# Kernel optimization log

Hardware: AMD Instinct MI355X
Metric: run time of the kernel (lower is better)

Reference implementation:

```python
import jax, jax.numpy as jnp
import numpy as np


def _gcn_conv(x, src, dst, W, b, n_nodes):
    """PyG GCNConv: out = D^-1/2 (A+I) D^-1/2 (x @ W) + b, sym norm with self-loops."""
    loop = jnp.arange(n_nodes, dtype=src.dtype)
    s = jnp.concatenate([src, loop])  # sources incl self-loops
    d = jnp.concatenate([dst, loop])  # destinations incl self-loops
    ones = jnp.ones(d.shape[0], dtype=x.dtype)
    deg = jax.ops.segment_sum(ones, d, num_segments=n_nodes)
    dinv = jnp.where(deg > 0, jax.lax.rsqrt(deg), 0.0)
    norm = dinv[s] * dinv[d]  # [E+N]
    h = x @ W  # dense transform first (in>=out channels), [N, H]
    msg = h[s] * norm[:, None]  # gather + scale, [E+N, H]
    out = jax.ops.segment_sum(msg, d, num_segments=n_nodes)  # scatter-add
    return out + b


def setup_inputs() -> dict:
    N, E, C_IN, C_H = 50000, 640000, 128, 128
    key = jax.random.key(0)
    k_x, k_e, k_w1, k_w2 = jax.random.split(key, 4)
    x = jax.random.normal(k_x, (N, C_IN), dtype=jnp.float32)
    edge_index = jax.random.randint(k_e, (2, E), 0, N, dtype=jnp.int64)
    # Glorot-style init for GCN weights, zero bias (PyG defaults)
    W1 = jax.random.normal(k_w1, (C_IN, C_H), dtype=jnp.float32) * (1.0 / np.sqrt(C_IN))
    b1 = jnp.zeros((C_H,), dtype=jnp.float32)
    W2 = jax.random.normal(k_w2, (C_H, C_H), dtype=jnp.float32) * (1.0 / np.sqrt(C_H))
    b2 = jnp.zeros((C_H,), dtype=jnp.float32)
    return {"x": x, "edge_index": edge_index, "W1": W1, "b1": b1, "W2": W2, "b2": b2}


def reference(x, edge_index, W1, b1, W2, b2):
    n_nodes = x.shape[0]
    src, dst = edge_index[0], edge_index[1]
    h = jax.nn.relu(_gcn_conv(x, src, dst, W1, b1, n_nodes))
    # dropout p=0.5 is identity in eval mode (training=False)
    h = jax.nn.relu(_gcn_conv(h, src, dst, W2, b2, n_nodes))
    return h
```

## Files before the change

### kernel.cpp

```cpp
#include <hip/hip_runtime.h>
#include <hip/hip_bf16.h>
#include <cstdint>

#define CH 128
#define NB 512
#define SCHUNK 4096

typedef __attribute__((ext_vector_type(8))) short short8;
typedef __attribute__((ext_vector_type(4))) float f32x4;

union FragU {
  uint4 u;
  short8 s;
  ushort h[8];
};

__device__ __forceinline__ float bf_lo(uint32_t u) { return __uint_as_float(u << 16); }
__device__ __forceinline__ float bf_hi(uint32_t u) { return __uint_as_float(u & 0xffff0000u); }
__device__ __forceinline__ uint32_t f2bf(float f) {
  uint32_t u = __float_as_uint(f);
  u += 0x7fff + ((u >> 16) & 1);
  return u >> 16;
}

__global__ __launch_bounds__(256) void k_hist2(const int* __restrict__ dst, int* __restrict__ counts,
                                               int E, int nblk) {
  __shared__ int sh[NB];
  int t = threadIdx.x, blk = blockIdx.x;
  for (int i = t; i < NB; i += 256) sh[i] = 0;
  __syncthreads();
  int base = blk * SCHUNK, lim = min(base + SCHUNK, E);
  for (int i = base + t; i < lim; i += 256) atomicAdd(&sh[dst[i] >> 7], 1);
  __syncthreads();
  for (int i = t; i < NB; i += 256) counts[i * nblk + blk] = sh[i];
}

__global__ __launch_bounds__(1024) void k_scan1(const int* __restrict__ in, int* __restrict__ excl,
                                                int* __restrict__ blocksum, int n) {
  __shared__ int sd[1024];
  int tid = threadIdx.x;
  int i = blockIdx.x * 1024 + tid;
  int v = (i < n) ? in[i] : 0;
  int x = v;
  sd[tid] = x;
  __syncthreads();
  for (int off = 1; off < 1024; off <<= 1) {
    int t = (tid >= off) ? sd[tid - off] : 0;
    __syncthreads();
    x += t;
    sd[tid] = x;
    __syncthreads();
  }
  if (i < n) excl[i] = x - v;
  if (tid == 1023) blocksum[blockIdx.x] = x;
}

__global__ void k_scan2b(int* __restrict__ bs, int nb) {
  __shared__ int sh[128];
  int t = threadIdx.x;
  int v = (t < nb) ? bs[t] : 0;
  sh[t] = v;
  __syncthreads();
  for (int off = 1; off < 128; off <<= 1) {
    int add = (t >= off) ? sh[t - off] : 0;
    __syncthreads();
    sh[t] += add;
    __syncthreads();
  }
  if (t < nb) bs[t] = sh[t] - v;
}

__global__ __launch_bounds__(256) void k_scan3b(int* __restrict__ excl, const int* __restrict__ boff,
                                                int* __restrict__ bbase, int total, int nblk, int E) {
  int i = blockIdx.x * 256 + threadIdx.x;
  if (i < total) {
    int val = excl[i] + boff[i >> 10];
    excl[i] = val;
    if (i % nblk == 0) bbase[i / nblk] = val;
  }
  if (i == 0) bbase[NB] = E;
}

__global__ __launch_bounds__(256) void k_scatter3(const int* __restrict__ src, const int* __restrict__ dst,
                                                  const int* __restrict__ excl, uint32_t* __restrict__ packed,
                                                  int E, int nblk) {
  __shared__ int lcur[NB];
  int t = threadIdx.x, blk = blockIdx.x;
  for (int i = t; i < NB; i += 256) lcur[i] = excl[i * nblk + blk];
  __syncthreads();
  int base = blk * SCHUNK, lim = min(base + SCHUNK, E);
  for (int i = base + t; i < lim; i += 256) {
    int d = dst[i], s = src[i];
    int slot = atomicAdd(&lcur[d >> 7], 1);
    packed[slot] = (uint32_t)s | ((uint32_t)(d & 127) << 16);
  }
}

__global__ __launch_bounds__(256) void k_bucket(const uint32_t* __restrict__ packed, const int* __restrict__ bbase,
                                                int* __restrict__ csr_src, int* __restrict__ row_ptr,
                                                float* __restrict__ dinv, int N, int E, int nb) {
  __shared__ int hist[128];
  __shared__ int scan[128];
  __shared__ int cur[128];
  int b = blockIdx.x;
  int t = threadIdx.x;
  int base = bbase[b], end = bbase[b + 1];
  if (t < 128) hist[t] = 0;
  __syncthreads();
  for (int i = base + t; i < end; i += 256)
    atomicAdd(&hist[packed[i] >> 16], 1);
  __syncthreads();
  int v = (t < 128) ? hist[t] : 0;
  if (t < 128) scan[t] = v;
  __syncthreads();
  for (int off = 1; off < 128; off <<= 1) {
    int add = (t < 128 && t >= off) ? scan[t - off] : 0;
    __syncthreads();
    if (t < 128) scan[t] += add;
    __syncthreads();
  }
  if (t < 128) {
    int excl = scan[t] - v;
    cur[t] = excl;
    int node = b * 128 + t;
    if (node < N) {
      row_ptr[node] = base + excl;
      dinv[node] = rsqrtf((float)(v + 1));
    }
    if (b == nb - 1 && t == 0) row_ptr[N] = E;
  }
  __syncthreads();
  for (int i = base + t; i < end; i += 256) {
    uint32_t p = packed[i];
    int slot = atomicAdd(&cur[p >> 16], 1);
    csr_src[base + slot] = (int)(p & 0xffffu);
  }
}

__global__ __launch_bounds__(256) void k_wpack(const float* __restrict__ W1, const float* __restrict__ W2,
                                               ushort* __restrict__ buf) {
  int which = blockIdx.x >> 6;
  int idx = (blockIdx.x & 63) * 256 + threadIdx.x;
  const float* W = which ? W2 : W1;
  ushort* hi = buf + which * 32768;
  ushort* lo = hi + 16384;
  int k = idx >> 7, n = idx & 127;
  float w = W[idx];
  uint32_t hb = f2bf(w);
  uint32_t lb = f2bf(w - bf_lo(hb));
  int j = n >> 4, t = k >> 5, ln = (n & 15) | (((k >> 3) & 3) << 4), i = k & 7;
  int p = (j * 4 + t) * 512 + ln * 8 + i;
  hi[p] = (ushort)hb;
  lo[p] = (ushort)lb;
}

template <typename TA, bool OUT_BF16>
__global__ __launch_bounds__(256) void k_gemm_mfma(const TA* __restrict__ A,
                                                   const ushort* __restrict__ wpack,
                                                   void* __restrict__ Cp, int n) {
  const int lane = threadIdx.x & 63;
  const int gwave = (blockIdx.x * 256 + threadIdx.x) >> 6;
  const int rb = gwave * 32;
  if (rb >= n) return;
  const int lrow = lane & 15, lgrp = lane >> 4;
  const uint4* whi4 = (const uint4*)wpack;
  const uint4* wlo4 = (const uint4*)(wpack + 16384);

  const int r0 = rb + lrow, r1 = rb + 16 + lrow;
  const bool v0 = r0 < n, v1 = r1 < n;
  const int rc0 = v0 ? r0 : 0, rc1 = v1 ? r1 : 0;

  f32x4 acc0[8] = {};
  f32x4 acc1[8] = {};
  const uint4 zz = make_uint4(0, 0, 0, 0);

#pragma unroll
  for (int t = 0; t < 4; ++t) {
    FragU a0h, a0l, a1h, a1l;
    if constexpr (sizeof(TA) == 4) {
      const float* ap0 = (const float*)A + (size_t)rc0 * CH + t * 32 + lgrp * 8;
      const float* ap1 = (const float*)A + (size_t)rc1 * CH + t * 32 + lgrp * 8;
      float4 xa = *(const float4*)ap0, xb = *(const float4*)(ap0 + 4);
      float4 ya = *(const float4*)ap1, yb = *(const float4*)(ap1 + 4);
      float xv[8] = {xa.x, xa.y, xa.z, xa.w, xb.x, xb.y, xb.z, xb.w};
      float yv[8] = {ya.x, ya.y, ya.z, ya.w, yb.x, yb.y, yb.z, yb.w};
#pragma unroll
      for (int i = 0; i < 8; ++i) {
        uint32_t h0 = f2bf(xv[i]);
        a0h.h[i] = (ushort)h0;
        a0l.h[i] = (ushort)f2bf(xv[i] - bf_lo(h0));
        uint32_t h1 = f2bf(yv[i]);
        a1h.h[i] = (ushort)h1;
        a1l.h[i] = (ushort)f2bf(yv[i] - bf_lo(h1));
      }
      if (!v0) { a0h.u = zz; a0l.u = zz; }
      if (!v1) { a1h.u = zz; a1l.u = zz; }
    } else {
      a0h.u = v0 ? *(const uint4*)((const ushort*)A + (size_t)rc0 * CH + t * 32 + lgrp * 8) : zz;
      a1h.u = v1 ? *(const uint4*)((const ushort*)A + (size_t)rc1 * CH + t * 32 + lgrp * 8) : zz;
    }
#pragma unroll
    for (int j = 0; j < 8; ++j) {
      FragU wh, wl;
      wh.u = whi4[(j * 4 + t) * 64 + lane];
      wl.u = wlo4[(j * 4 + t) * 64 + lane];
      acc0[j] = __builtin_amdgcn_mfma_f32_16x16x32_bf16(wh.s, a0h.s, acc0[j], 0, 0, 0);
      acc0[j] = __builtin_amdgcn_mfma_f32_16x16x32_bf16(wl.s, a0h.s, acc0[j], 0, 0, 0);
      acc1[j] = __builtin_amdgcn_mfma_f32_16x16x32_bf16(wh.s, a1h.s, acc1[j], 0, 0, 0);
      acc1[j] = __builtin_amdgcn_mfma_f32_16x16x32_bf16(wl.s, a1h.s, acc1[j], 0, 0, 0);
      if constexpr (sizeof(TA) == 4) {
        acc0[j] = __builtin_amdgcn_mfma_f32_16x16x32_bf16(wh.s, a0l.s, acc0[j], 0, 0, 0);
        acc1[j] = __builtin_amdgcn_mfma_f32_16x16x32_bf16(wh.s, a1l.s, acc1[j], 0, 0, 0);
      }
    }
  }

  if (v0) {
#pragma unroll
    for (int j = 0; j < 8; ++j) {
      if constexpr (OUT_BF16) {
        uint2 o;
        o.x = f2bf(acc0[j][0]) | (f2bf(acc0[j][1]) << 16);
        o.y = f2bf(acc0[j][2]) | (f2bf(acc0[j][3]) << 16);
        *(uint2*)&((ushort*)Cp)[(size_t)r0 * CH + j * 16 + lgrp * 4] = o;
      } else {
        float4 o = make_float4(acc0[j][0], acc0[j][1], acc0[j][2], acc0[j][3]);
        *(float4*)&((float*)Cp)[(size_t)r0 * CH + j * 16 + lgrp * 4] = o;
      }
    }
  }
  if (v1) {
#pragma unroll
    for (int j = 0; j < 8; ++j) {
      if constexpr (OUT_BF16) {
        uint2 o;
        o.x = f2bf(acc1[j][0]) | (f2bf(acc1[j][1]) << 16);
        o.y = f2bf(acc1[j][2]) | (f2bf(acc1[j][3]) << 16);
        *(uint2*)&((ushort*)Cp)[(size_t)r1 * CH + j * 16 + lgrp * 4] = o;
      } else {
        float4 o = make_float4(acc1[j][0], acc1[j][1], acc1[j][2], acc1[j][3]);
        *(float4*)&((float*)Cp)[(size_t)r1 * CH + j * 16 + lgrp * 4] = o;
      }
    }
  }
}

template <bool OUT_BF16>
__global__ __launch_bounds__(256) void k_agg(const ushort* __restrict__ h, const int* __restrict__ row_ptr,
                                             const int* __restrict__ csr_src, const float* __restrict__ dinv,
                                             const float* __restrict__ b, void* __restrict__ outp, int n) {
  int v = (blockIdx.x * 256 + threadIdx.x) >> 6;
  int lane = threadIdx.x & 63;
  if (v >= n) return;
  v = __builtin_amdgcn_readfirstlane(v);
  float dv = dinv[v];
  uint32_t us = *(const uint32_t*)&h[(size_t)v * CH + 2 * lane];
  float self = dv * dv;
  float acc0 = bf_lo(us) * self;
  float acc1 = bf_hi(us) * self;
  int j = row_ptr[v], end = row_ptr[v + 1];
  for (; j + 3 < end; j += 4) {
    int s0 = csr_src[j], s1 = csr_src[j + 1], s2 = csr_src[j + 2], s3 = csr_src[j + 3];
    float w0 = dinv[s0] * dv, w1 = dinv[s1] * dv, w2 = dinv[s2] * dv, w3 = dinv[s3] * dv;
    uint32_t u0 = *(const uint32_t*)&h[(size_t)s0 * CH + 2 * lane];
    uint32_t u1 = *(const uint32_t*)&h[(size_t)s1 * CH + 2 * lane];
    uint32_t u2 = *(const uint32_t*)&h[(size_t)s2 * CH + 2 * lane];
    uint32_t u3 = *(const uint32_t*)&h[(size_t)s3 * CH + 2 * lane];
    acc0 += bf_lo(u0) * w0; acc1 += bf_hi(u0) * w0;
    acc0 += bf_lo(u1) * w1; acc1 += bf_hi(u1) * w1;
    acc0 += bf_lo(u2) * w2; acc1 += bf_hi(u2) * w2;
    acc0 += bf_lo(u3) * w3; acc1 += bf_hi(u3) * w3;
  }
  for (; j < end; ++j) {
    int s0 = csr_src[j];
    float w0 = dinv[s0] * dv;
    uint32_t u0 = *(const uint32_t*)&h[(size_t)s0 * CH + 2 * lane];
    acc0 += bf_lo(u0) * w0; acc1 += bf_hi(u0) * w0;
  }
  float2 bb = *(const float2*)&b[2 * lane];
  acc0 = fmaxf(acc0 + bb.x, 0.f);
  acc1 = fmaxf(acc1 + bb.y, 0.f);
  if constexpr (OUT_BF16) {
    ((uint32_t*)outp)[(size_t)v * 64 + lane] = f2bf(acc0) | (f2bf(acc1) << 16);
  } else {
    ((float2*)outp)[(size_t)v * 64 + lane] = make_float2(acc0, acc1);
  }
}


extern "C" void kernel_launch(void* const* d_in, const int* in_sizes, int n_in,
                              void* d_out, int out_size, void* d_ws, size_t ws_size,
                              hipStream_t stream) {
  const float* x  = (const float*)d_in[0];
  const int*   ei = (const int*)d_in[1];
  const float* W1 = (const float*)d_in[2];
  const float* b1 = (const float*)d_in[3];
  const float* W2 = (const float*)d_in[4];
  const float* b2 = (const float*)d_in[5];
  float* out = (float*)d_out;

  const int N = in_sizes[0] / CH;
  const int E = in_sizes[1] / 2;
  const int* src = ei;
  const int* dst = ei + E;
  const int nb = (N + 127) / 128;
  const int nblk = (E + SCHUNK - 1) / SCHUNK;
  const int total = NB * nblk;
  const int nsb = (total + 1023) / 1024;

  char* ws = (char*)d_ws;
  size_t off = 0;
  auto alloc = [&](size_t bytes) -> void* {
    void* p = ws + off;
    off += (bytes + 255) & ~(size_t)255;
    return p;
  };
  int*      counts  = (int*)alloc((size_t)total * 4);
  int*      blocksum= (int*)alloc(128 * 4);
  int*      bbase   = (int*)alloc((NB + 1) * 4);
  uint32_t* packed  = (uint32_t*)alloc((size_t)E * 4);
  int*      row_ptr = (int*)alloc((size_t)(N + 1) * 4);
  int*      csr_src = (int*)alloc((size_t)E * 4);
  float*    dinv    = (float*)alloc((size_t)N * 4);
  ushort*   wpack   = (ushort*)alloc(4 * 16384 * 2);
  ushort*   h       = (ushort*)alloc((size_t)N * CH * 2);
  ushort*   y1      = (ushort*)alloc((size_t)N * CH * 2);
  (void)ws_size;

  k_hist2<<<nblk, 256, 0, stream>>>(dst, counts, E, nblk);
  k_scan1<<<nsb, 1024, 0, stream>>>(counts, counts, blocksum, total);
  k_scan2b<<<1, 128, 0, stream>>>(blocksum, nsb);
  k_scan3b<<<(total + 255) / 256, 256, 0, stream>>>(counts, blocksum, bbase, total, nblk, E);
  k_scatter3<<<nblk, 256, 0, stream>>>(src, dst, counts, packed, E, nblk);
  k_bucket<<<nb, 256, 0, stream>>>(packed, bbase, csr_src, row_ptr, dinv, N, E, nb);
  k_wpack<<<128, 256, 0, stream>>>(W1, W2, wpack);

  const int waves = (N + 31) / 32;
  const int gG = (waves + 3) / 4;
  const int gA = (N + 3) / 4;

  k_gemm_mfma<float, true><<<gG, 256, 0, stream>>>(x, wpack, h, N);
  k_agg<true><<<gA, 256, 0, stream>>>(h, row_ptr, csr_src, dinv, b1, y1, N);
  k_gemm_mfma<ushort, true><<<gG, 256, 0, stream>>>(y1, wpack + 32768, h, N);
  k_agg<false><<<gA, 256, 0, stream>>>(h, row_ptr, csr_src, dinv, b2, out, N);
}
```

Measured before the change: 131.8 us.

## Fuse layer-1 aggregation with layer-2 GEMM, prescale by dinv, merge prep kernels

Fuses the first aggregation with the second GEMM through shared memory, so the intermediate y1 never goes to global memory and one launch disappears. The GEMM epilogue now multiplies rows by dinv, which removes the per-edge dinv gather in aggregation; the aggregation loop is unrolled by 8 with wave-uniform bounds. The three scan kernels become a single-block scan, and weight packing is merged into the histogram launch. Risks: the fused kernel has only 32 nodes per block, so aggregation latency may be exposed, and the single-block scan is serial per thread.

```diff
diff --git a/kernel.cpp b/kernel.cpp
--- a/kernel.cpp
+++ b/kernel.cpp
@@ -23,10 +23,30 @@
   return u >> 16;
 }
 
-__global__ __launch_bounds__(256) void k_hist2(const int* __restrict__ dst, int* __restrict__ counts,
-                                               int E, int nblk) {
+__global__ __launch_bounds__(256) void k_histw(const int* __restrict__ dst, int* __restrict__ counts,
+                                               int E, int nblk,
+                                               const float* __restrict__ W1, const float* __restrict__ W2,
+                                               ushort* __restrict__ wbuf) {
+  int blk = blockIdx.x;
+  if (blk >= nblk) {
+    int bb = blk - nblk;
+    int which = bb >> 6;
+    int idx = (bb & 63) * 256 + threadIdx.x;
+    const float* W = which ? W2 : W1;
+    ushort* hi = wbuf + which * 32768;
+    ushort* lo = hi + 16384;
+    int k = idx >> 7, n = idx & 127;
+    float w = W[idx];
+    uint32_t hb = f2bf(w);
+    uint32_t lb = f2bf(w - bf_lo(hb));
+    int j = n >> 4, t = k >> 5, ln = (n & 15) | (((k >> 3) & 3) << 4), i = k & 7;
+    int p = (j * 4 + t) * 512 + ln * 8 + i;
+    hi[p] = (ushort)hb;
+    lo[p] = (ushort)lb;
+    return;
+  }
   __shared__ int sh[NB];
-  int t = threadIdx.x, blk = blockIdx.x;
+  int t = threadIdx.x;
   for (int i = t; i < NB; i += 256) sh[i] = 0;
   __syncthreads();
   int base = blk * SCHUNK, lim = min(base + SCHUNK, E);
@@ -35,50 +55,30 @@
   for (int i = t; i < NB; i += 256) counts[i * nblk + blk] = sh[i];
 }
 
-__global__ __launch_bounds__(1024) void k_scan1(const int* __restrict__ in, int* __restrict__ excl,
-                                                int* __restrict__ blocksum, int n) {
-  __shared__ int sd[1024];
-  int tid = threadIdx.x;
-  int i = blockIdx.x * 1024 + tid;
-  int v = (i < n) ? in[i] : 0;
-  int x = v;
-  sd[tid] = x;
+__global__ __launch_bounds__(1024) void k_scan_all(int* __restrict__ counts, int* __restrict__ bbase,
+                                                   int total, int nblk, int E) {
+  __shared__ int ssum[1024];
+  int t = threadIdx.x;
+  int chunk = (total + 1023) / 1024;
+  int lo = t * chunk, hi = min(lo + chunk, total);
+  int s = 0;
+  for (int i = lo; i < hi; ++i) s += counts[i];
+  ssum[t] = s;
   __syncthreads();
   for (int off = 1; off < 1024; off <<= 1) {
-    int t = (tid >= off) ? sd[tid - off] : 0;
+    int add = (t >= off) ? ssum[t - off] : 0;
     __syncthreads();
-    x += t;
-    sd[tid] = x;
+    ssum[t] += add;
     __syncthreads();
   }
-  if (i < n) excl[i] = x - v;
-  if (tid == 1023) blocksum[blockIdx.x] = x;
-}
-
-__global__ void k_scan2b(int* __restrict__ bs, int nb) {
-  __shared__ int sh[128];
-  int t = threadIdx.x;
-  int v = (t < nb) ? bs[t] : 0;
-  sh[t] = v;
-  __syncthreads();
-  for (int off = 1; off < 128; off <<= 1) {
-    int add = (t >= off) ? sh[t - off] : 0;
-    __syncthreads();
-    sh[t] += add;
-    __syncthreads();
-  }
-  if (t < nb) bs[t] = sh[t] - v;
-}
-
-__global__ __launch_bounds__(256) void k_scan3b(int* __restrict__ excl, const int* __restrict__ boff,
-                                                int* __restrict__ bbase, int total, int nblk, int E) {
-  int i = blockIdx.x * 256 + threadIdx.x;
-  if (i < total) {
-    int val = excl[i] + boff[i >> 10];
-    excl[i] = val;
-    if (i % nblk == 0) bbase[i / nblk] = val;
-  }
-  if (i == 0) bbase[NB] = E;
+  int run = ssum[t] - s;
+  for (int i = lo; i < hi; ++i) {
+    int v = counts[i];
+    counts[i] = run;
+    if (i % nblk == 0) bbase[i / nblk] = run;
+    run += v;
+  }
+  if (t == 0) bbase[NB] = E;
 }
 
 __global__ __launch_bounds__(256) void k_scatter3(const int* __restrict__ src, const int* __restrict__ dst,
@@ -137,27 +137,10 @@
   }
 }
 
-__global__ __launch_bounds__(256) void k_wpack(const float* __restrict__ W1, const float* __restrict__ W2,
-                                               ushort* __restrict__ buf) {
-  int which = blockIdx.x >> 6;
-  int idx = (blockIdx.x & 63) * 256 + threadIdx.x;
-  const float* W = which ? W2 : W1;
-  ushort* hi = buf + which * 32768;
-  ushort* lo = hi + 16384;
-  int k = idx >> 7, n = idx & 127;
-  float w = W[idx];
-  uint32_t hb = f2bf(w);
-  uint32_t lb = f2bf(w - bf_lo(hb));
-  int j = n >> 4, t = k >> 5, ln = (n & 15) | (((k >> 3) & 3) << 4), i = k & 7;
-  int p = (j * 4 + t) * 512 + ln * 8 + i;
-  hi[p] = (ushort)hb;
-  lo[p] = (ushort)lb;
-}
-
-template <typename TA, bool OUT_BF16>
-__global__ __launch_bounds__(256) void k_gemm_mfma(const TA* __restrict__ A,
+__global__ __launch_bounds__(256) void k_gemm_mfma(const float* __restrict__ A,
                                                    const ushort* __restrict__ wpack,
-                                                   void* __restrict__ Cp, int n) {
+                                                   const float* __restrict__ dinv,
+                                                   ushort* __restrict__ Cp, int n) {
   const int lane = threadIdx.x & 63;
   const int gwave = (blockIdx.x * 256 + threadIdx.x) >> 6;
   const int rb = gwave * 32;
@@ -177,28 +160,23 @@
 #pragma unroll
   for (int t = 0; t < 4; ++t) {
     FragU a0h, a0l, a1h, a1l;
-    if constexpr (sizeof(TA) == 4) {
-      const float* ap0 = (const float*)A + (size_t)rc0 * CH + t * 32 + lgrp * 8;
-      const float* ap1 = (const float*)A + (size_t)rc1 * CH + t * 32 + lgrp * 8;
-      float4 xa = *(const float4*)ap0, xb = *(const float4*)(ap0 + 4);
-      float4 ya = *(const float4*)ap1, yb = *(const float4*)(ap1 + 4);
-      float xv[8] = {xa.x, xa.y, xa.z, xa.w, xb.x, xb.y, xb.z, xb.w};
-      float yv[8] = {ya.x, ya.y, ya.z, ya.w, yb.x, yb.y, yb.z, yb.w};
-#pragma unroll
-      for (int i = 0; i < 8; ++i) {
-        uint32_t h0 = f2bf(xv[i]);
-        a0h.h[i] = (ushort)h0;
-        a0l.h[i] = (ushort)f2bf(xv[i] - bf_lo(h0));
-        uint32_t h1 = f2bf(yv[i]);
-        a1h.h[i] = (ushort)h1;
-        a1l.h[i] = (ushort)f2bf(yv[i] - bf_lo(h1));
-      }
-      if (!v0) { a0h.u = zz; a0l.u = zz; }
-      if (!v1) { a1h.u = zz; a1l.u = zz; }
-    } else {
-      a0h.u = v0 ? *(const uint4*)((const ushort*)A + (size_t)rc0 * CH + t * 32 + lgrp * 8) : zz;
-      a1h.u = v1 ? *(const uint4*)((const ushort*)A + (size_t)rc1 * CH + t * 32 + lgrp * 8) : zz;
-    }
+    const float* ap0 = A + (size_t)rc0 * CH + t * 32 + lgrp * 8;
+    const float* ap1 = A + (size_t)rc1 * CH + t * 32 + lgrp * 8;
+    float4 xa = *(const float4*)ap0, xb = *(const float4*)(ap0 + 4);
+    float4 ya = *(const float4*)ap1, yb = *(const float4*)(ap1 + 4);
+    float xv[8] = {xa.x, xa.y, xa.z, xa.w, xb.x, xb.y, xb.z, xb.w};
+    float yv[8] = {ya.x, ya.y, ya.z, ya.w, yb.x, yb.y, yb.z, yb.w};
+#pragma unroll
+    for (int i = 0; i < 8; ++i) {
+      uint32_t h0 = f2bf(xv[i]);
+      a0h.h[i] = (ushort)h0;
+      a0l.h[i] = (ushort)f2bf(xv[i] - bf_lo(h0));
+      uint32_t h1 = f2bf(yv[i]);
+      a1h.h[i] = (ushort)h1;
+      a1l.h[i] = (ushort)f2bf(yv[i] - bf_lo(h1));
+    }
+    if (!v0) { a0h.u = zz; a0l.u = zz; }
+    if (!v1) { a1h.u = zz; a1l.u = zz; }
 #pragma unroll
     for (int j = 0; j < 8; ++j) {
       FragU wh, wl;
@@ -206,85 +184,149 @@
       wl.u = wlo4[(j * 4 + t) * 64 + lane];
       acc0[j] = __builtin_amdgcn_mfma_f32_16x16x32_bf16(wh.s, a0h.s, acc0[j], 0, 0, 0);
       acc0[j] = __builtin_amdgcn_mfma_f32_16x16x32_bf16(wl.s, a0h.s, acc0[j], 0, 0, 0);
+      acc0[j] = __builtin_amdgcn_mfma_f32_16x16x32_bf16(wh.s, a0l.s, acc0[j], 0, 0, 0);
       acc1[j] = __builtin_amdgcn_mfma_f32_16x16x32_bf16(wh.s, a1h.s, acc1[j], 0, 0, 0);
       acc1[j] = __builtin_amdgcn_mfma_f32_16x16x32_bf16(wl.s, a1h.s, acc1[j], 0, 0, 0);
-      if constexpr (sizeof(TA) == 4) {
-        acc0[j] = __builtin_amdgcn_mfma_f32_16x16x32_bf16(wh.s, a0l.s, acc0[j], 0, 0, 0);
-        acc1[j] = __builtin_amdgcn_mfma_f32_16x16x32_bf16(wh.s, a1l.s, acc1[j], 0, 0, 0);
+      acc1[j] = __builtin_amdgcn_mfma_f32_16x16x32_bf16(wh.s, a1l.s, acc1[j], 0, 0, 0);
+    }
+  }
+
+  if (v0) {
+    float dv = dinv[r0];
+#pragma unroll
+    for (int j = 0; j < 8; ++j) {
+      uint2 o;
+      o.x = f2bf(acc0[j][0] * dv) | (f2bf(acc0[j][1] * dv) << 16);
+      o.y = f2bf(acc0[j][2] * dv) | (f2bf(acc0[j][3] * dv) << 16);
+      *(uint2*)&Cp[(size_t)r0 * CH + j * 16 + lgrp * 4] = o;
+    }
+  }
+  if (v1) {
+    float dv = dinv[r1];
+#pragma unroll
+    for (int j = 0; j < 8; ++j) {
+      uint2 o;
+      o.x = f2bf(acc1[j][0] * dv) | (f2bf(acc1[j][1] * dv) << 16);
+      o.y = f2bf(acc1[j][2] * dv) | (f2bf(acc1[j][3] * dv) << 16);
+      *(uint2*)&Cp[(size_t)r1 * CH + j * 16 + lgrp * 4] = o;
+    }
+  }
+}
+
+__device__ __forceinline__ void agg_node(const uint32_t* __restrict__ hp, const int* __restrict__ row_ptr,
+                                         const int* __restrict__ csr, int v, int lane,
+                                         float& a0, float& a1) {
+  uint32_t self = hp[(size_t)v * 64 + lane];
+  float acc0 = bf_lo(self), acc1 = bf_hi(self);
+  int j = __builtin_amdgcn_readfirstlane(row_ptr[v]);
+  int end = __builtin_amdgcn_readfirstlane(row_ptr[v + 1]);
+  for (; j + 7 < end; j += 8) {
+    int s[8];
+#pragma unroll
+    for (int k = 0; k < 8; ++k) s[k] = csr[j + k];
+    uint32_t u[8];
+#pragma unroll
+    for (int k = 0; k < 8; ++k) u[k] = hp[(size_t)s[k] * 64 + lane];
+#pragma unroll
+    for (int k = 0; k < 8; ++k) { acc0 += bf_lo(u[k]); acc1 += bf_hi(u[k]); }
+  }
+  for (; j < end; ++j) {
+    uint32_t u = hp[(size_t)csr[j] * 64 + lane];
+    acc0 += bf_lo(u); acc1 += bf_hi(u);
+  }
+  a0 = acc0;
+  a1 = acc1;
+}
+
+__global__ __launch_bounds__(256) void k_fused(const uint32_t* __restrict__ h1p, const int* __restrict__ row_ptr,
+                                               const int* __restrict__ csr, const float* __restrict__ dinv,
+                                               const float* __restrict__ b1,
+                                               const ushort* __restrict__ wpack2,
+                                               ushort* __restrict__ h2, int N) {
+  __shared__ uint32_t sy[32 * 64];
+  const int w = threadIdx.x >> 6;
+  const int lane = threadIdx.x & 63;
+  const int vb = blockIdx.x * 32;
+  float2 bb = *(const float2*)&b1[2 * lane];
+
+  for (int q = 0; q < 8; ++q) {
+    int lv = w * 8 + q;
+    int v = vb + lv;
+    uint32_t packed = 0;
+    if (v < N) {
+      float a0, a1;
+      agg_node(h1p, row_ptr, csr, v, lane, a0, a1);
+      float dv = dinv[v];
+      float o0 = fmaxf(fmaf(dv, a0, bb.x), 0.f);
+      float o1 = fmaxf(fmaf(dv, a1, bb.y), 0.f);
+      packed = f2bf(o0) | (f2bf(o1) << 16);
+    }
+    sy[lv * 64 + (lane ^ ((lv & 7) << 2))] = packed;
+  }
+  __syncthreads();
+
+  const int lrow = lane & 15, lgrp = lane >> 4;
+  const uint4* whi4 = (const uint4*)wpack2;
+  const uint4* wlo4 = (const uint4*)(wpack2 + 16384);
+
+  FragU af[2][4];
+#pragma unroll
+  for (int rt = 0; rt < 2; ++rt) {
+#pragma unroll
+    for (int t = 0; t < 4; ++t) {
+      int row = rt * 16 + lrow;
+      int grp = (t * 4 + lgrp) ^ (row & 7);
+      af[rt][t].u = *(const uint4*)&sy[row * 64 + grp * 4];
+    }
+  }
+
+  f32x4 acc[2][2] = {};
+#pragma unroll
+  for (int jj = 0; jj < 2; ++jj) {
+    int j = w * 2 + jj;
+#pragma unroll
+    for (int t = 0; t < 4; ++t) {
+      FragU wh, wl;
+      wh.u = whi4[(j * 4 + t) * 64 + lane];
+      wl.u = wlo4[(j * 4 + t) * 64 + lane];
+      acc[0][jj] = __builtin_amdgcn_mfma_f32_16x16x32_bf16(wh.s, af[0][t].s, acc[0][jj], 0, 0, 0);
+      acc[0][jj] = __builtin_amdgcn_mfma_f32_16x16x32_bf16(wl.s, af[0][t].s, acc[0][jj], 0, 0, 0);
+      acc[1][jj] = __builtin_amdgcn_mfma_f32_16x16x32_bf16(wh.s, af[1][t].s, acc[1][jj], 0, 0, 0);
+      acc[1][jj] = __builtin_amdgcn_mfma_f32_16x16x32_bf16(wl.s, af[1][t].s, acc[1][jj], 0, 0, 0);
+    }
+  }
+
+#pragma unroll
+  for (int rt = 0; rt < 2; ++rt) {
+    int r = vb + rt * 16 + lrow;
+    if (r < N) {
+      float dvr = dinv[r];
+#pragma unroll
+      for (int jj = 0; jj < 2; ++jj) {
+        int j = w * 2 + jj;
+        uint2 o;
+        o.x = f2bf(acc[rt][jj][0] * dvr) | (f2bf(acc[rt][jj][1] * dvr) << 16);
+        o.y = f2bf(acc[rt][jj][2] * dvr) | (f2bf(acc[rt][jj][3] * dvr) << 16);
+        *(uint2*)&h2[(size_t)r * CH + j * 16 + lgrp * 4] = o;
       }
     }
   }
-
-  if (v0) {
-#pragma unroll
-    for (int j = 0; j < 8; ++j) {
-      if constexpr (OUT_BF16) {
-        uint2 o;
-        o.x = f2bf(acc0[j][0]) | (f2bf(acc0[j][1]) << 16);
-        o.y = f2bf(acc0[j][2]) | (f2bf(acc0[j][3]) << 16);
-        *(uint2*)&((ushort*)Cp)[(size_t)r0 * CH + j * 16 + lgrp * 4] = o;
-      } else {
-        float4 o = make_float4(acc0[j][0], acc0[j][1], acc0[j][2], acc0[j][3]);
-        *(float4*)&((float*)Cp)[(size_t)r0 * CH + j * 16 + lgrp * 4] = o;
-      }
-    }
-  }
-  if (v1) {
-#pragma unroll
-    for (int j = 0; j < 8; ++j) {
-      if constexpr (OUT_BF16) {
-        uint2 o;
-        o.x = f2bf(acc1[j][0]) | (f2bf(acc1[j][1]) << 16);
-        o.y = f2bf(acc1[j][2]) | (f2bf(acc1[j][3]) << 16);
-        *(uint2*)&((ushort*)Cp)[(size_t)r1 * CH + j * 16 + lgrp * 4] = o;
-      } else {
-        float4 o = make_float4(acc1[j][0], acc1[j][1], acc1[j][2], acc1[j][3]);
-        *(float4*)&((float*)Cp)[(size_t)r1 * CH + j * 16 + lgrp * 4] = o;
-      }
-    }
-  }
-}
-
-template <bool OUT_BF16>
-__global__ __launch_bounds__(256) void k_agg(const ushort* __restrict__ h, const int* __restrict__ row_ptr,
-                                             const int* __restrict__ csr_src, const float* __restrict__ dinv,
-                                             const float* __restrict__ b, void* __restrict__ outp, int n) {
+}
+
+__global__ __launch_bounds__(256) void k_agg2(const uint32_t* __restrict__ h2p, const int* __restrict__ row_ptr,
+                                              const int* __restrict__ csr, const float* __restrict__ dinv,
+                                              const float* __restrict__ b2, float* __restrict__ out, int n) {
   int v = (blockIdx.x * 256 + threadIdx.x) >> 6;
   int lane = threadIdx.x & 63;
   if (v >= n) return;
   v = __builtin_amdgcn_readfirstlane(v);
+  float a0, a1;
+  agg_node(h2p, row_ptr, csr, v, lane, a0, a1);
   float dv = dinv[v];
-  uint32_t us = *(const uint32_t*)&h[(size_t)v * CH + 2 * lane];
-  float self = dv * dv;
-  float acc0 = bf_lo(us) * self;
-  float acc1 = bf_hi(us) * self;
-  int j = row_ptr[v], end = row_ptr[v + 1];
-  for (; j + 3 < end; j += 4) {
-    int s0 = csr_src[j], s1 = csr_src[j + 1], s2 = csr_src[j + 2], s3 = csr_src[j + 3];
-    float w0 = dinv[s0] * dv, w1 = dinv[s1] * dv, w2 = dinv[s2] * dv, w3 = dinv[s3] * dv;
-    uint32_t u0 = *(const uint32_t*)&h[(size_t)s0 * CH + 2 * lane];
-    uint32_t u1 = *(const uint32_t*)&h[(size_t)s1 * CH + 2 * lane];
-    uint32_t u2 = *(const uint32_t*)&h[(size_t)s2 * CH + 2 * lane];
-    uint32_t u3 = *(const uint32_t*)&h[(size_t)s3 * CH + 2 * lane];
-    acc0 += bf_lo(u0) * w0; acc1 += bf_hi(u0) * w0;
-    acc0 += bf_lo(u1) * w1; acc1 += bf_hi(u1) * w1;
-    acc0 += bf_lo(u2) * w2; acc1 += bf_hi(u2) * w2;
-    acc0 += bf_lo(u3) * w3; acc1 += bf_hi(u3) * w3;
-  }
-  for (; j < end; ++j) {
-    int s0 = csr_src[j];
-    float w0 = dinv[s0] * dv;
-    uint32_t u0 = *(const uint32_t*)&h[(size_t)s0 * CH + 2 * lane];
-    acc0 += bf_lo(u0) * w0; acc1 += bf_hi(u0) * w0;
-  }
-  float2 bb = *(const float2*)&b[2 * lane];
-  acc0 = fmaxf(acc0 + bb.x, 0.f);
-  acc1 = fmaxf(acc1 + bb.y, 0.f);
-  if constexpr (OUT_BF16) {
-    ((uint32_t*)outp)[(size_t)v * 64 + lane] = f2bf(acc0) | (f2bf(acc1) << 16);
-  } else {
-    ((float2*)outp)[(size_t)v * 64 + lane] = make_float2(acc0, acc1);
-  }
+  float2 bb = *(const float2*)&b2[2 * lane];
+  float o0 = fmaxf(fmaf(dv, a0, bb.x), 0.f);
+  float o1 = fmaxf(fmaf(dv, a1, bb.y), 0.f);
+  ((float2*)out)[(size_t)v * 64 + lane] = make_float2(o0, o1);
 }
 
 
@@ -306,7 +348,6 @@
   const int nb = (N + 127) / 128;
   const int nblk = (E + SCHUNK - 1) / SCHUNK;
   const int total = NB * nblk;
-  const int nsb = (total + 1023) / 1024;
 
   char* ws = (char*)d_ws;
   size_t off = 0;
@@ -316,31 +357,28 @@
     return p;
   };
   int*      counts  = (int*)alloc((size_t)total * 4);
-  int*      blocksum= (int*)alloc(128 * 4);
   int*      bbase   = (int*)alloc((NB + 1) * 4);
   uint32_t* packed  = (uint32_t*)alloc((size_t)E * 4);
   int*      row_ptr = (int*)alloc((size_t)(N + 1) * 4);
   int*      csr_src = (int*)alloc((size_t)E * 4);
   float*    dinv    = (float*)alloc((size_t)N * 4);
   ushort*   wpack   = (ushort*)alloc(4 * 16384 * 2);
-  ushort*   h       = (ushort*)alloc((size_t)N * CH * 2);
-  ushort*   y1      = (ushort*)alloc((size_t)N * CH * 2);
+  ushort*   h1      = (ushort*)alloc((size_t)N * CH * 2);
+  ushort*   h2      = (ushort*)alloc((size_t)N * CH * 2);
   (void)ws_size;
 
-  k_hist2<<<nblk, 256, 0, stream>>>(dst, counts, E, nblk);
-  k_scan1<<<nsb, 1024, 0, stream>>>(counts, counts, blocksum, total);
-  k_scan2b<<<1, 128, 0, stream>>>(blocksum, nsb);
-  k_scan3b<<<(total + 255) / 256, 256, 0, stream>>>(counts, blocksum, bbase, total, nblk, E);
+  k_histw<<<nblk + 128, 256, 0, stream>>>(dst, counts, E, nblk, W1, W2, wpack);
+  k_scan_all<<<1, 1024, 0, stream>>>(counts, bbase, total, nblk, E);
   k_scatter3<<<nblk, 256, 0, stream>>>(src, dst, counts, packed, E, nblk);
   k_bucket<<<nb, 256, 0, stream>>>(packed, bbase, csr_src, row_ptr, dinv, N, E, nb);
-  k_wpack<<<128, 256, 0, stream>>>(W1, W2, wpack);
 
   const int waves = (N + 31) / 32;
   const int gG = (waves + 3) / 4;
+  const int gF = (N + 31) / 32;
   const int gA = (N + 3) / 4;
 
-  k_gemm_mfma<float, true><<<gG, 256, 0, stream>>>(x, wpack, h, N);
-  k_agg<true><<<gA, 256, 0, stream>>>(h, row_ptr, csr_src, dinv, b1, y1, N);
-  k_gemm_mfma<ushort, true><<<gG, 256, 0, stream>>>(y1, wpack + 32768, h, N);
-  k_agg<false><<<gA, 256, 0, stream>>>(h, row_ptr, csr_src, dinv, b2, out, N);
-}
+  k_gemm_mfma<<<gG, 256, 0, stream>>>(x, wpack, dinv, h1, N);
+  k_fused<<<gF, 256, 0, stream>>>((const uint32_t*)h1, row_ptr, csr_src, dinv, b1,
+                                  wpack + 32768, h2, N);
+  k_agg2<<<gA, 256, 0, stream>>>((const uint32_t*)h2, row_ptr, csr_src, dinv, b2, out, N);
+}
```

Result: slower. 236.0 us (+79.0%).
